# Kernel tuning notes

Measured on AMD Instinct MI355X. Metric: run time of the kernel, lower is better.

## Reference

```python
import jax, jax.numpy as jnp
import numpy as np

B, S, D = 32, 256, 128
K = 16          # num_sample (negatives + the positive appended last)
V = 50000       # vocab / num_classes


def setup_inputs() -> dict:
    key = jax.random.key(0)
    k1, k2, k3, k4 = jax.random.split(key, 4)
    return {
        "input_latent": jax.random.normal(k1, (B, S, D), dtype=jnp.float32),
        "target_labels": jax.random.randint(k2, (B, S), 0, V, dtype=jnp.int64),
        "batch_samples": jax.random.randint(k3, (B, S * (K - 1)), 0, V, dtype=jnp.int64),
        "embed_weight": jax.random.normal(k4, (V, D), dtype=jnp.float32),
    }


def reference(input_latent, target_labels, batch_samples, embed_weight):
    b, s, d = input_latent.shape
    out_emb = embed_weight[target_labels]                      # [B,S,D] positives
    neg_emb = embed_weight[batch_samples].reshape(b, s, K - 1, d)
    # Candidates per target position j: K-1 negatives + the positive itself (last)
    samples = jnp.concatenate([neg_emb, out_emb[:, :, None, :]], axis=2)  # [B,S,K,D]
    # sample_rep[b,i,j,k] = latent[b,i] . samples[b,j,k]
    sample_scores = jnp.einsum('bid,bjkd->bijk', input_latent, samples)   # [B,S,S,K]
    # output_rep[b,i,j] = latent[b,i] . out_emb[b,j] (== sample_scores[...,K-1])
    out_scores = jnp.einsum('bid,bjd->bij', input_latent, out_emb)        # [B,S,S]
    # log( exp(out - max) / sum_k exp(sample - max) ) = out - logsumexp(sample)
    lse = jax.scipy.special.logsumexp(sample_scores, axis=3)              # [B,S,S]
    return out_scores - lse
```

## Files before the change

### kernel.cpp

```cpp
#include <hip/hip_runtime.h>
#include <hip/hip_bf16.h>
#include <math.h>

#define BB 32
#define SS 256
#define DD 128
#define KK 16
#define VV 50000
#define SK (SS*KK)
#define LOG2E 1.44269504f
#define LN2   0.69314718f

typedef __attribute__((ext_vector_type(8))) short bf16x8;
typedef __attribute__((ext_vector_type(4))) float f32x4;
typedef __attribute__((ext_vector_type(16))) float f32x16;
typedef unsigned short ushort_t;

static __device__ __forceinline__ short f2bf(float f) {
    __hip_bfloat16 h = __float2bfloat16(f);
    return *(short*)&h;
}

static __device__ __forceinline__ float fast_exp2(float x) {
    float r; asm("v_exp_f32 %0, %1" : "=v"(r) : "v"(x)); return r;
}
static __device__ __forceinline__ float fast_log2(float x) {
    float r; asm("v_log_f32 %0, %1" : "=v"(r) : "v"(x)); return r;
}

static __device__ __forceinline__ int lds_off(int row, int d) {
    return row * 256 + ((d * 2) ^ ((row & 15) << 4));
}

__global__ __launch_bounds__(256, 2)
void neg_loss_persist(const float* __restrict__ latent,
                      const int*   __restrict__ labels,
                      const int*   __restrict__ samples,
                      const float* __restrict__ embed,
                      float* __restrict__ out)
{
    __shared__ char  ldsA[SS * 256];
    __shared__ float trans[256][9];

    const int p     = blockIdx.x;
    const int b     = p >> 4;
    const int npair = p & 15;
    const int tid   = threadIdx.x;
    const int wave  = tid >> 6;
    const int lane  = tid & 63;
    const int l31   = lane & 31;
    const int hi    = lane >> 5;

    const int rB  = wave * 32 + l31;
    const int gc0 = (npair * 2) * 128 + rB;
    const int gc1 = gc0 + 128;
    const int j0i = gc0 >> 4, k0i = gc0 & 15;
    const int j1i = gc1 >> 4, k1i = gc1 & 15;
    const int idx0 = (k0i < 15)
        ? samples[(size_t)b * (SS * (KK - 1)) + j0i * (KK - 1) + k0i]
        : labels[b * SS + j0i];
    const int idx1 = (k1i < 15)
        ? samples[(size_t)b * (SS * (KK - 1)) + j1i * (KK - 1) + k1i]
        : labels[b * SS + j1i];

    f32x4 fbA[16];
    {
        const float* rowp = embed + (size_t)idx0 * DD + hi * 8;
        #pragma unroll
        for (int ks = 0; ks < 8; ++ks) {
            fbA[2 * ks]     = *(const f32x4*)(rowp + ks * 16);
            fbA[2 * ks + 1] = *(const f32x4*)(rowp + ks * 16 + 4);
        }
    }

    #pragma unroll
    for (int pr = 0; pr < 4; ++pr) {
        const int r  = pr * 64 + (tid >> 2);
        const int d0 = (tid & 3) * 32;
        const float* src = latent + ((size_t)b * SS + r) * DD + d0;
        f32x4 f[8];
        #pragma unroll
        for (int c = 0; c < 8; ++c) f[c] = *(const f32x4*)(src + 4 * c);
        short o[32];
        #pragma unroll
        for (int c = 0; c < 8; ++c)
            #pragma unroll
            for (int e = 0; e < 4; ++e)
                o[4 * c + e] = f2bf(f[c][e] * LOG2E);
        #pragma unroll
        for (int c = 0; c < 4; ++c)
            *(bf16x8*)(ldsA + lds_off(r, d0 + 8 * c)) = *(bf16x8*)(o + 8 * c);
    }

    __syncthreads();

    f32x4 fbB[16];
    {
        const float* rowp = embed + (size_t)idx1 * DD + hi * 8;
        #pragma unroll
        for (int ks = 0; ks < 8; ++ks) {
            fbB[2 * ks]     = *(const f32x4*)(rowp + ks * 16);
            fbB[2 * ks + 1] = *(const f32x4*)(rowp + ks * 16 + 4);
        }
    }

    #pragma unroll
    for (int t = 0; t < 2; ++t) {
        const int tile_n = npair * 2 + t;
        const int jc     = wave * 2 + hi;

        bf16x8 av[8];
        #pragma unroll
        for (int ks = 0; ks < 8; ++ks) {
            const f32x4 lo = t ? fbB[2 * ks]     : fbA[2 * ks];
            const f32x4 hi4 = t ? fbB[2 * ks + 1] : fbA[2 * ks + 1];
            short t8[8];
            #pragma unroll
            for (int e = 0; e < 4; ++e) t8[e]     = f2bf(lo[e]);
            #pragma unroll
            for (int e = 0; e < 4; ++e) t8[4 + e] = f2bf(hi4[e]);
            av[ks] = *(bf16x8*)t8;
        }

        f32x16 acc[4][2] = {};
        #pragma unroll
        for (int ks = 0; ks < 8; ++ks) {
            const int d = ks * 16 + hi * 8;
            #pragma unroll
            for (int mt = 0; mt < 4; ++mt) {
                bf16x8 bv0 = *(const bf16x8*)(ldsA + lds_off(mt * 64 + l31, d));
                bf16x8 bv1 = *(const bf16x8*)(ldsA + lds_off(mt * 64 + 32 + l31, d));
                acc[mt][0] = __builtin_amdgcn_mfma_f32_32x32x16_bf16(av[ks], bv0, acc[mt][0], 0, 0, 0);
                acc[mt][1] = __builtin_amdgcn_mfma_f32_32x32x16_bf16(av[ks], bv1, acc[mt][1], 0, 0, 0);
            }
        }

        #pragma unroll
        for (int mt = 0; mt < 4; ++mt) {
            #pragma unroll
            for (int f = 0; f < 2; ++f) {
                const f32x16 v = acc[mt][f];
                float pm0 = fmaxf(fmaxf(fmaxf(v[0], v[1]), fmaxf(v[2], v[3])),
                                  fmaxf(fmaxf(v[4], v[5]), fmaxf(v[6], v[7])));
                float pm1 = fmaxf(fmaxf(fmaxf(v[8], v[9]), fmaxf(v[10], v[11])),
                                  fmaxf(fmaxf(v[12], v[13]), fmaxf(v[14], v[15])));
                float om0 = fmaxf(pm0, __shfl_xor(pm0, 32));
                float om1 = fmaxf(pm1, __shfl_xor(pm1, 32));
                float e0 = ((fast_exp2(v[0] - om0) + fast_exp2(v[1] - om0))
                          + (fast_exp2(v[2] - om0) + fast_exp2(v[3] - om0)))
                         + ((fast_exp2(v[4] - om0) + fast_exp2(v[5] - om0))
                          + (fast_exp2(v[6] - om0) + fast_exp2(v[7] - om0)));
                float e1 = ((fast_exp2(v[8]  - om1) + fast_exp2(v[9]  - om1))
                          + (fast_exp2(v[10] - om1) + fast_exp2(v[11] - om1)))
                         + ((fast_exp2(v[12] - om1) + fast_exp2(v[13] - om1))
                          + (fast_exp2(v[14] - om1) + fast_exp2(v[15] - om1)));
                float s0 = e0 + __shfl_xor(e0, 32);
                float s1 = e1 + __shfl_xor(e1, 32);
                float pos0 = __shfl_xor(v[7], 32);
                float pos1 = v[15];
                const float pos = hi ? pos1 : pos0;
                const float om  = hi ? om1  : om0;
                const float s   = hi ? s1   : s0;
                const int i = mt * 64 + f * 32 + l31;
                trans[i][jc] = (pos - om - fast_log2(s)) * LN2;
            }
        }

        __syncthreads();

        {
            const int i = tid;
            float r[8];
            #pragma unroll
            for (int c = 0; c < 8; ++c) r[c] = trans[i][c];
            float* dst = out + ((size_t)b * SS + i) * SS + tile_n * 8;
            *(f32x4*)(dst)     = *(f32x4*)(r);
            *(f32x4*)(dst + 4) = *(f32x4*)(r + 4);
        }

        if (t == 0) __syncthreads();
    }
}

extern "C" void kernel_launch(void* const* d_in, const int* in_sizes, int n_in,
                              void* d_out, int out_size, void* d_ws, size_t ws_size,
                              hipStream_t stream) {
    const float* latent  = (const float*)d_in[0];
    const int*   labels  = (const int*)d_in[1];
    const int*   samples = (const int*)d_in[2];
    const float* embed   = (const float*)d_in[3];
    float* out = (float*)d_out;

    neg_loss_persist<<<dim3(512), dim3(256), 0, stream>>>(
        latent, labels, samples, embed, out);
}
```

Before: 32.55 us.

## Split work into smaller 128x128 tiles over a 3D grid for more blocks

Replaces the persistent 512-block kernel, which processed two column tiles over all 256 rows, with a 2048-block grid where each block computes one 128-row by 128-candidate tile. LDS use is halved and launch bounds allow three blocks per CU, raising occupancy and parallelism to hide gather and MFMA latency. In exchange, latent rows are loaded and converted twice as often and embedding rows are gathered once per row-half. The manual prefetch overlap of the second tile's gather is also lost.

Measured after the change: 40.64 us. 1.25x slower.

```diff
diff --git a/kernel.cpp b/kernel.cpp
--- a/kernel.cpp
+++ b/kernel.cpp
@@ -14,7 +14,6 @@
 typedef __attribute__((ext_vector_type(8))) short bf16x8;
 typedef __attribute__((ext_vector_type(4))) float f32x4;
 typedef __attribute__((ext_vector_type(16))) float f32x16;
-typedef unsigned short ushort_t;
 
 static __device__ __forceinline__ short f2bf(float f) {
     __hip_bfloat16 h = __float2bfloat16(f);
@@ -32,52 +31,50 @@
     return row * 256 + ((d * 2) ^ ((row & 15) << 4));
 }
 
-__global__ __launch_bounds__(256, 2)
-void neg_loss_persist(const float* __restrict__ latent,
-                      const int*   __restrict__ labels,
-                      const int*   __restrict__ samples,
-                      const float* __restrict__ embed,
-                      float* __restrict__ out)
+__global__ __launch_bounds__(256, 3)
+void neg_loss_main(const float* __restrict__ latent,
+                   const int*   __restrict__ labels,
+                   const int*   __restrict__ samples,
+                   const float* __restrict__ embed,
+                   float* __restrict__ out)
 {
-    __shared__ char  ldsA[SS * 256];
-    __shared__ float trans[256][9];
+    __shared__ char  ldsA[128 * 256];
+    __shared__ float trans[128][9];
 
-    const int p     = blockIdx.x;
-    const int b     = p >> 4;
-    const int npair = p & 15;
-    const int tid   = threadIdx.x;
-    const int wave  = tid >> 6;
-    const int lane  = tid & 63;
-    const int l31   = lane & 31;
-    const int hi    = lane >> 5;
+    const int nt   = blockIdx.x;
+    const int mh   = blockIdx.y;
+    const int b    = blockIdx.z;
+    const int n0   = nt * 128;
+    const int m0   = mh * 128;
+    const int tid  = threadIdx.x;
+    const int wave = tid >> 6;
+    const int lane = tid & 63;
+    const int l31  = lane & 31;
+    const int hi   = lane >> 5;
 
     const int rB  = wave * 32 + l31;
-    const int gc0 = (npair * 2) * 128 + rB;
-    const int gc1 = gc0 + 128;
-    const int j0i = gc0 >> 4, k0i = gc0 & 15;
-    const int j1i = gc1 >> 4, k1i = gc1 & 15;
-    const int idx0 = (k0i < 15)
-        ? samples[(size_t)b * (SS * (KK - 1)) + j0i * (KK - 1) + k0i]
-        : labels[b * SS + j0i];
-    const int idx1 = (k1i < 15)
-        ? samples[(size_t)b * (SS * (KK - 1)) + j1i * (KK - 1) + k1i]
-        : labels[b * SS + j1i];
+    const int gc  = n0 + rB;
+    const int j   = gc >> 4;
+    const int k   = gc & 15;
+    const int idx = (k < 15)
+        ? samples[(size_t)b * (SS * (KK - 1)) + j * (KK - 1) + k]
+        : labels[b * SS + j];
 
-    f32x4 fbA[16];
+    f32x4 fb[16];
     {
-        const float* rowp = embed + (size_t)idx0 * DD + hi * 8;
+        const float* rowp = embed + (size_t)idx * DD + hi * 8;
         #pragma unroll
         for (int ks = 0; ks < 8; ++ks) {
-            fbA[2 * ks]     = *(const f32x4*)(rowp + ks * 16);
-            fbA[2 * ks + 1] = *(const f32x4*)(rowp + ks * 16 + 4);
+            fb[2 * ks]     = *(const f32x4*)(rowp + ks * 16);
+            fb[2 * ks + 1] = *(const f32x4*)(rowp + ks * 16 + 4);
         }
     }
 
     #pragma unroll
-    for (int pr = 0; pr < 4; ++pr) {
+    for (int pr = 0; pr < 2; ++pr) {
         const int r  = pr * 64 + (tid >> 2);
         const int d0 = (tid & 3) * 32;
-        const float* src = latent + ((size_t)b * SS + r) * DD + d0;
+        const float* src = latent + ((size_t)b * SS + m0 + r) * DD + d0;
         f32x4 f[8];
         #pragma unroll
         for (int c = 0; c < 8; ++c) f[c] = *(const f32x4*)(src + 4 * c);
@@ -94,91 +91,72 @@
 
     __syncthreads();
 
-    f32x4 fbB[16];
-    {
-        const float* rowp = embed + (size_t)idx1 * DD + hi * 8;
+    bf16x8 av[8];
+    #pragma unroll
+    for (int ks = 0; ks < 8; ++ks) {
+        short t8[8];
         #pragma unroll
-        for (int ks = 0; ks < 8; ++ks) {
-            fbB[2 * ks]     = *(const f32x4*)(rowp + ks * 16);
-            fbB[2 * ks + 1] = *(const f32x4*)(rowp + ks * 16 + 4);
+        for (int e = 0; e < 4; ++e) t8[e]     = f2bf(fb[2 * ks][e]);
+        #pragma unroll
+        for (int e = 0; e < 4; ++e) t8[4 + e] = f2bf(fb[2 * ks + 1][e]);
+        av[ks] = *(bf16x8*)t8;
+    }
+
+    f32x16 acc[2][2] = {};
+    #pragma unroll
+    for (int ks = 0; ks < 8; ++ks) {
+        const int d = ks * 16 + hi * 8;
+        #pragma unroll
+        for (int mt = 0; mt < 2; ++mt) {
+            bf16x8 bv0 = *(const bf16x8*)(ldsA + lds_off(mt * 64 + l31, d));
+            bf16x8 bv1 = *(const bf16x8*)(ldsA + lds_off(mt * 64 + 32 + l31, d));
+            acc[mt][0] = __builtin_amdgcn_mfma_f32_32x32x16_bf16(av[ks], bv0, acc[mt][0], 0, 0, 0);
+            acc[mt][1] = __builtin_amdgcn_mfma_f32_32x32x16_bf16(av[ks], bv1, acc[mt][1], 0, 0, 0);
         }
     }
 
+    const int jc = wave * 2 + hi;
     #pragma unroll
-    for (int t = 0; t < 2; ++t) {
-        const int tile_n = npair * 2 + t;
-        const int jc     = wave * 2 + hi;
+    for (int mt = 0; mt < 2; ++mt) {
+        #pragma unroll
+        for (int f = 0; f < 2; ++f) {
+            const f32x16 v = acc[mt][f];
+            float pm0 = fmaxf(fmaxf(fmaxf(v[0], v[1]), fmaxf(v[2], v[3])),
+                              fmaxf(fmaxf(v[4], v[5]), fmaxf(v[6], v[7])));
+            float pm1 = fmaxf(fmaxf(fmaxf(v[8], v[9]), fmaxf(v[10], v[11])),
+                              fmaxf(fmaxf(v[12], v[13]), fmaxf(v[14], v[15])));
+            float om0 = fmaxf(pm0, __shfl_xor(pm0, 32));
+            float om1 = fmaxf(pm1, __shfl_xor(pm1, 32));
+            float e0 = ((fast_exp2(v[0] - om0) + fast_exp2(v[1] - om0))
+                      + (fast_exp2(v[2] - om0) + fast_exp2(v[3] - om0)))
+                     + ((fast_exp2(v[4] - om0) + fast_exp2(v[5] - om0))
+                      + (fast_exp2(v[6] - om0) + fast_exp2(v[7] - om0)));
+            float e1 = ((fast_exp2(v[8]  - om1) + fast_exp2(v[9]  - om1))
+                      + (fast_exp2(v[10] - om1) + fast_exp2(v[11] - om1)))
+                     + ((fast_exp2(v[12] - om1) + fast_exp2(v[13] - om1))
+                      + (fast_exp2(v[14] - om1) + fast_exp2(v[15] - om1)));
+            float s0 = e0 + __shfl_xor(e0, 32);
+            float s1 = e1 + __shfl_xor(e1, 32);
+            float pos0 = __shfl_xor(v[7], 32);
+            float pos1 = v[15];
+            const float pos = hi ? pos1 : pos0;
+            const float om  = hi ? om1  : om0;
+            const float s   = hi ? s1   : s0;
+            const int i = mt * 64 + f * 32 + l31;
+            trans[i][jc] = (pos - om - fast_log2(s)) * LN2;
+        }
+    }
 
-        bf16x8 av[8];
+    __syncthreads();
+
+    if (tid < 128) {
+        const int i = tid;
+        float r[8];
         #pragma unroll
-        for (int ks = 0; ks < 8; ++ks) {
-            const f32x4 lo = t ? fbB[2 * ks]     : fbA[2 * ks];
-            const f32x4 hi4 = t ? fbB[2 * ks + 1] : fbA[2 * ks + 1];
-            short t8[8];
-            #pragma unroll
-            for (int e = 0; e < 4; ++e) t8[e]     = f2bf(lo[e]);
-            #pragma unroll
-            for (int e = 0; e < 4; ++e) t8[4 + e] = f2bf(hi4[e]);
-            av[ks] = *(bf16x8*)t8;
-        }
-
-        f32x16 acc[4][2] = {};
-        #pragma unroll
-        for (int ks = 0; ks < 8; ++ks) {
-            const int d = ks * 16 + hi * 8;
-            #pragma unroll
-            for (int mt = 0; mt < 4; ++mt) {
-                bf16x8 bv0 = *(const bf16x8*)(ldsA + lds_off(mt * 64 + l31, d));
-                bf16x8 bv1 = *(const bf16x8*)(ldsA + lds_off(mt * 64 + 32 + l31, d));
-                acc[mt][0] = __builtin_amdgcn_mfma_f32_32x32x16_bf16(av[ks], bv0, acc[mt][0], 0, 0, 0);
-                acc[mt][1] = __builtin_amdgcn_mfma_f32_32x32x16_bf16(av[ks], bv1, acc[mt][1], 0, 0, 0);
-            }
-        }
-
-        #pragma unroll
-        for (int mt = 0; mt < 4; ++mt) {
-            #pragma unroll
-            for (int f = 0; f < 2; ++f) {
-                const f32x16 v = acc[mt][f];
-                float pm0 = fmaxf(fmaxf(fmaxf(v[0], v[1]), fmaxf(v[2], v[3])),
-                                  fmaxf(fmaxf(v[4], v[5]), fmaxf(v[6], v[7])));
-                float pm1 = fmaxf(fmaxf(fmaxf(v[8], v[9]), fmaxf(v[10], v[11])),
-                                  fmaxf(fmaxf(v[12], v[13]), fmaxf(v[14], v[15])));
-                float om0 = fmaxf(pm0, __shfl_xor(pm0, 32));
-                float om1 = fmaxf(pm1, __shfl_xor(pm1, 32));
-                float e0 = ((fast_exp2(v[0] - om0) + fast_exp2(v[1] - om0))
-                          + (fast_exp2(v[2] - om0) + fast_exp2(v[3] - om0)))
-                         + ((fast_exp2(v[4] - om0) + fast_exp2(v[5] - om0))
-                          + (fast_exp2(v[6] - om0) + fast_exp2(v[7] - om0)));
-                float e1 = ((fast_exp2(v[8]  - om1) + fast_exp2(v[9]  - om1))
-                          + (fast_exp2(v[10] - om1) + fast_exp2(v[11] - om1)))
-                         + ((fast_exp2(v[12] - om1) + fast_exp2(v[13] - om1))
-                          + (fast_exp2(v[14] - om1) + fast_exp2(v[15] - om1)));
-                float s0 = e0 + __shfl_xor(e0, 32);
-                float s1 = e1 + __shfl_xor(e1, 32);
-                float pos0 = __shfl_xor(v[7], 32);
-                float pos1 = v[15];
-                const float pos = hi ? pos1 : pos0;
-                const float om  = hi ? om1  : om0;
-                const float s   = hi ? s1   : s0;
-                const int i = mt * 64 + f * 32 + l31;
-                trans[i][jc] = (pos - om - fast_log2(s)) * LN2;
-            }
-        }
-
-        __syncthreads();
-
-        {
-            const int i = tid;
-            float r[8];
-            #pragma unroll
-            for (int c = 0; c < 8; ++c) r[c] = trans[i][c];
-            float* dst = out + ((size_t)b * SS + i) * SS + tile_n * 8;
-            *(f32x4*)(dst)     = *(f32x4*)(r);
-            *(f32x4*)(dst + 4) = *(f32x4*)(r + 4);
-        }
-
-        if (t == 0) __syncthreads();
+        for (int c = 0; c < 8; ++c) r[c] = trans[i][c];
+        float* dst = out + ((size_t)b * SS + m0 + i) * SS + nt * 8;
+        *(f32x4*)(dst)     = *(f32x4*)(r);
+        *(f32x4*)(dst + 4) = *(f32x4*)(r + 4);
     }
 }
 
@@ -191,6 +169,6 @@
     const float* embed   = (const float*)d_in[3];
     float* out = (float*)d_out;
 
-    neg_loss_persist<<<dim3(512), dim3(256), 0, stream>>>(
+    neg_loss_main<<<dim3(32, 2, 32), dim3(256), 0, stream>>>(
         latent, labels, samples, embed, out);
 }
```

## Pre-convert latent to bf16 in a workspace and load into LDS directly

Applied to the files above, without the earlier changes.

Adds a pre-pass kernel that converts the fp32 latent to bf16 scaled by log2(e) in the workspace. The main kernel then fills its swizzled LDS tile with global_load_lds DMA instead of loading, converting and storing through registers. Each of the 16 blocks per batch previously repeated that conversion; the cost of removing it is an extra kernel launch and a workspace round trip. The original fused kernel is kept as a fallback when the workspace is too small.

New measurement: 32.36 us (median of 2 runs). About the same (-0.6%).

```diff
diff --git a/kernel.cpp b/kernel.cpp
--- a/kernel.cpp
+++ b/kernel.cpp
@@ -32,8 +32,33 @@
     return row * 256 + ((d * 2) ^ ((row & 15) << 4));
 }
 
+static __device__ __forceinline__ void gload_lds16(const void* g, void* lds) {
+    __builtin_amdgcn_global_load_lds(
+        (const __attribute__((address_space(1))) unsigned int*)g,
+        (__attribute__((address_space(3))) unsigned int*)lds, 16, 0, 0);
+}
+
+#define NLAT (BB*SS*DD)
+#define NCHUNK_LAT (NLAT/8)
+
+__global__ __launch_bounds__(256)
+void convert_lat_kernel(const float* __restrict__ latent,
+                        ushort_t* __restrict__ ws_lat)
+{
+    int i = blockIdx.x * 256 + threadIdx.x;
+    if (i >= NCHUNK_LAT) return;
+    const float* src = latent + (size_t)i * 8;
+    float f[8];
+    *(f32x4*)(f + 0) = ((const f32x4*)src)[0];
+    *(f32x4*)(f + 4) = ((const f32x4*)src)[1];
+    short o[8];
+    #pragma unroll
+    for (int e = 0; e < 8; ++e) o[e] = f2bf(f[e] * LOG2E);
+    *(bf16x8*)(ws_lat + (size_t)i * 8) = *(bf16x8*)o;
+}
+
 __global__ __launch_bounds__(256, 2)
-void neg_loss_persist(const float* __restrict__ latent,
+void neg_loss_persist(const ushort_t* __restrict__ lat_bf,
                       const int*   __restrict__ labels,
                       const int*   __restrict__ samples,
                       const float* __restrict__ embed,
@@ -48,6 +73,8 @@
     const int tid   = threadIdx.x;
     const int wave  = tid >> 6;
     const int lane  = tid & 63;
+    const int q     = lane & 15;
+    const int sub   = lane >> 4;
     const int l31   = lane & 31;
     const int hi    = lane >> 5;
 
@@ -74,22 +101,12 @@
     }
 
     #pragma unroll
-    for (int pr = 0; pr < 4; ++pr) {
-        const int r  = pr * 64 + (tid >> 2);
-        const int d0 = (tid & 3) * 32;
-        const float* src = latent + ((size_t)b * SS + r) * DD + d0;
-        f32x4 f[8];
-        #pragma unroll
-        for (int c = 0; c < 8; ++c) f[c] = *(const f32x4*)(src + 4 * c);
-        short o[32];
-        #pragma unroll
-        for (int c = 0; c < 8; ++c)
-            #pragma unroll
-            for (int e = 0; e < 4; ++e)
-                o[4 * c + e] = f2bf(f[c][e] * LOG2E);
-        #pragma unroll
-        for (int c = 0; c < 4; ++c)
-            *(bf16x8*)(ldsA + lds_off(r, d0 + 8 * c)) = *(bf16x8*)(o + 8 * c);
+    for (int t = 0; t < 16; ++t) {
+        const int r0 = wave * 64 + t * 4;
+        const int r  = r0 + sub;
+        const ushort_t* src = lat_bf + ((size_t)(b * SS + r) * DD)
+                                     + ((q ^ (r & 15)) << 3);
+        gload_lds16(src, ldsA + r0 * 256);
     }
 
     __syncthreads();
@@ -112,7 +129,7 @@
         bf16x8 av[8];
         #pragma unroll
         for (int ks = 0; ks < 8; ++ks) {
-            const f32x4 lo = t ? fbB[2 * ks]     : fbA[2 * ks];
+            const f32x4 lo  = t ? fbB[2 * ks]     : fbA[2 * ks];
             const f32x4 hi4 = t ? fbB[2 * ks + 1] : fbA[2 * ks + 1];
             short t8[8];
             #pragma unroll
@@ -182,6 +199,156 @@
     }
 }
 
+__global__ __launch_bounds__(256, 2)
+void neg_loss_fused(const float* __restrict__ latent,
+                    const int*   __restrict__ labels,
+                    const int*   __restrict__ samples,
+                    const float* __restrict__ embed,
+                    float* __restrict__ out)
+{
+    __shared__ char  ldsA[SS * 256];
+    __shared__ float trans[256][9];
+
+    const int p     = blockIdx.x;
+    const int b     = p >> 4;
+    const int npair = p & 15;
+    const int tid   = threadIdx.x;
+    const int wave  = tid >> 6;
+    const int lane  = tid & 63;
+    const int l31   = lane & 31;
+    const int hi    = lane >> 5;
+
+    const int rB  = wave * 32 + l31;
+    const int gc0 = (npair * 2) * 128 + rB;
+    const int gc1 = gc0 + 128;
+    const int j0i = gc0 >> 4, k0i = gc0 & 15;
+    const int j1i = gc1 >> 4, k1i = gc1 & 15;
+    const int idx0 = (k0i < 15)
+        ? samples[(size_t)b * (SS * (KK - 1)) + j0i * (KK - 1) + k0i]
+        : labels[b * SS + j0i];
+    const int idx1 = (k1i < 15)
+        ? samples[(size_t)b * (SS * (KK - 1)) + j1i * (KK - 1) + k1i]
+        : labels[b * SS + j1i];
+
+    f32x4 fbA[16];
+    {
+        const float* rowp = embed + (size_t)idx0 * DD + hi * 8;
+        #pragma unroll
+        for (int ks = 0; ks < 8; ++ks) {
+            fbA[2 * ks]     = *(const f32x4*)(rowp + ks * 16);
+            fbA[2 * ks + 1] = *(const f32x4*)(rowp + ks * 16 + 4);
+        }
+    }
+
+    #pragma unroll
+    for (int pr = 0; pr < 4; ++pr) {
+        const int r  = pr * 64 + (tid >> 2);
+        const int d0 = (tid & 3) * 32;
+        const float* src = latent + ((size_t)b * SS + r) * DD + d0;
+        f32x4 f[8];
+        #pragma unroll
+        for (int c = 0; c < 8; ++c) f[c] = *(const f32x4*)(src + 4 * c);
+        short o[32];
+        #pragma unroll
+        for (int c = 0; c < 8; ++c)
+            #pragma unroll
+            for (int e = 0; e < 4; ++e)
+                o[4 * c + e] = f2bf(f[c][e] * LOG2E);
+        #pragma unroll
+        for (int c = 0; c < 4; ++c)
+            *(bf16x8*)(ldsA + lds_off(r, d0 + 8 * c)) = *(bf16x8*)(o + 8 * c);
+    }
+
+    __syncthreads();
+
+    f32x4 fbB[16];
+    {
+        const float* rowp = embed + (size_t)idx1 * DD + hi * 8;
+        #pragma unroll
+        for (int ks = 0; ks < 8; ++ks) {
+            fbB[2 * ks]     = *(const f32x4*)(rowp + ks * 16);
+            fbB[2 * ks + 1] = *(const f32x4*)(rowp + ks * 16 + 4);
+        }
+    }
+
+    #pragma unroll
+    for (int t = 0; t < 2; ++t) {
+        const int tile_n = npair * 2 + t;
+        const int jc     = wave * 2 + hi;
+
+        bf16x8 av[8];
+        #pragma unroll
+        for (int ks = 0; ks < 8; ++ks) {
+            const f32x4 lo  = t ? fbB[2 * ks]     : fbA[2 * ks];
+            const f32x4 hi4 = t ? fbB[2 * ks + 1] : fbA[2 * ks + 1];
+            short t8[8];
+            #pragma unroll
+            for (int e = 0; e < 4; ++e) t8[e]     = f2bf(lo[e]);
+            #pragma unroll
+            for (int e = 0; e < 4; ++e) t8[4 + e] = f2bf(hi4[e]);
+            av[ks] = *(bf16x8*)t8;
+        }
+
+        f32x16 acc[4][2] = {};
+        #pragma unroll
+        for (int ks = 0; ks < 8; ++ks) {
+            const int d = ks * 16 + hi * 8;
+            #pragma unroll
+            for (int mt = 0; mt < 4; ++mt) {
+                bf16x8 bv0 = *(const bf16x8*)(ldsA + lds_off(mt * 64 + l31, d));
+                bf16x8 bv1 = *(const bf16x8*)(ldsA + lds_off(mt * 64 + 32 + l31, d));
+                acc[mt][0] = __builtin_amdgcn_mfma_f32_32x32x16_bf16(av[ks], bv0, acc[mt][0], 0, 0, 0);
+                acc[mt][1] = __builtin_amdgcn_mfma_f32_32x32x16_bf16(av[ks], bv1, acc[mt][1], 0, 0, 0);
+            }
+        }
+
+        #pragma unroll
+        for (int mt = 0; mt < 4; ++mt) {
+            #pragma unroll
+            for (int f = 0; f < 2; ++f) {
+                const f32x16 v = acc[mt][f];
+                float pm0 = fmaxf(fmaxf(fmaxf(v[0], v[1]), fmaxf(v[2], v[3])),
+                                  fmaxf(fmaxf(v[4], v[5]), fmaxf(v[6], v[7])));
+                float pm1 = fmaxf(fmaxf(fmaxf(v[8], v[9]), fmaxf(v[10], v[11])),
+                                  fmaxf(fmaxf(v[12], v[13]), fmaxf(v[14], v[15])));
+                float om0 = fmaxf(pm0, __shfl_xor(pm0, 32));
+                float om1 = fmaxf(pm1, __shfl_xor(pm1, 32));
+                float e0 = ((fast_exp2(v[0] - om0) + fast_exp2(v[1] - om0))
+                          + (fast_exp2(v[2] - om0) + fast_exp2(v[3] - om0)))
+                         + ((fast_exp2(v[4] - om0) + fast_exp2(v[5] - om0))
+                          + (fast_exp2(v[6] - om0) + fast_exp2(v[7] - om0)));
+                float e1 = ((fast_exp2(v[8]  - om1) + fast_exp2(v[9]  - om1))
+                          + (fast_exp2(v[10] - om1) + fast_exp2(v[11] - om1)))
+                         + ((fast_exp2(v[12] - om1) + fast_exp2(v[13] - om1))
+                          + (fast_exp2(v[14] - om1) + fast_exp2(v[15] - om1)));
+                float s0 = e0 + __shfl_xor(e0, 32);
+                float s1 = e1 + __shfl_xor(e1, 32);
+                float pos0 = __shfl_xor(v[7], 32);
+                float pos1 = v[15];
+                const float pos = hi ? pos1 : pos0;
+                const float om  = hi ? om1  : om0;
+                const float s   = hi ? s1   : s0;
+                const int i = mt * 64 + f * 32 + l31;
+                trans[i][jc] = (pos - om - fast_log2(s)) * LN2;
+            }
+        }
+
+        __syncthreads();
+
+        {
+            const int i = tid;
+            float r[8];
+            #pragma unroll
+            for (int c = 0; c < 8; ++c) r[c] = trans[i][c];
+            float* dst = out + ((size_t)b * SS + i) * SS + tile_n * 8;
+            *(f32x4*)(dst)     = *(f32x4*)(r);
+            *(f32x4*)(dst + 4) = *(f32x4*)(r + 4);
+        }
+
+        if (t == 0) __syncthreads();
+    }
+}
+
 extern "C" void kernel_launch(void* const* d_in, const int* in_sizes, int n_in,
                               void* d_out, int out_size, void* d_ws, size_t ws_size,
                               hipStream_t stream) {
@@ -191,6 +358,14 @@
     const float* embed   = (const float*)d_in[3];
     float* out = (float*)d_out;
 
-    neg_loss_persist<<<dim3(512), dim3(256), 0, stream>>>(
-        latent, labels, samples, embed, out);
-}
+    if (ws_size >= (size_t)NLAT * 2) {
+        ushort_t* ws_lat = (ushort_t*)d_ws;
+        convert_lat_kernel<<<(NCHUNK_LAT + 255) / 256, 256, 0, stream>>>(
+            latent, ws_lat);
+        neg_loss_persist<<<dim3(512), dim3(256), 0, stream>>>(
+            ws_lat, labels, samples, embed, out);
+    } else {
+        neg_loss_fused<<<dim3(512), dim3(256), 0, stream>>>(
+            latent, labels, samples, embed, out);
+    }
+}
```
